# Kernel optimization log

Hardware: AMD Instinct MI355X
Metric: run time of the kernel (lower is better)

The kernel has to match this reference:

```python
import jax, jax.numpy as jnp
import numpy as np

QP = 127.0          # signed symmetric 8-bit: Qp = 2**(8-1)-1
MIN_RANGE = 1e-6


def _ste_round(q):
    # round_pass: straight-through estimator round
    return q + jax.lax.stop_gradient(jnp.round(q) - q)


def _quant_per_token(x):
    # symmetric per-token: amax over last dim, keepdim
    s = jnp.clip(jnp.max(jnp.abs(x), axis=-1, keepdims=True), MIN_RANGE, None) / QP
    return _ste_round(x / s), s


def _quant_per_tensor(w):
    s = jnp.clip(jnp.max(jnp.abs(w)), MIN_RANGE, None) / QP
    return _ste_round(w / s), s


def _qlinear(x2d, w, b):
    # fake-quant linear: quantize act per-token, weight per-tensor,
    # int-domain matmul, bias added before dequant rescale (faithful to source)
    qx, sx = _quant_per_token(x2d)      # [N,K], [N,1]
    qw, sw = _quant_per_tensor(w)       # [M,K], scalar
    out = jnp.matmul(qx, qw.T) + b[None, :]
    return out * (sx * sw)              # [N,M]


def setup_inputs() -> dict:
    key = jax.random.key(0)
    k1, k2, k3, k4, k5 = jax.random.split(key, 5)
    B, S, D, H = 64, 197, 768, 3072
    return {
        "x": jax.random.normal(k1, (B, S, D), dtype=jnp.float32),
        "w1": jax.random.normal(k2, (H, D), dtype=jnp.float32) * 0.02,
        "b1": jax.random.normal(k3, (H,), dtype=jnp.float32) * 0.02,
        "w2": jax.random.normal(k4, (D, H), dtype=jnp.float32) * 0.02,
        "b2": jax.random.normal(k5, (D,), dtype=jnp.float32) * 0.02,
    }


def reference(x, w1, b1, w2, b2):
    B, S, D = x.shape
    x2d = x.reshape(-1, D)                         # view(-1, x.size(-1))
    h = _qlinear(x2d, w1, b1)                      # fc1
    h = jax.nn.gelu(h, approximate=False)          # ViT Mlp activation (exact GELU)
    o = _qlinear(h, w2, b2)                        # fc2
    return o.reshape(B, S, -1)
```

## Files before the change

### kernel.cpp

```cpp
#include <hip/hip_runtime.h>
#include <stdint.h>

#define QPF  127.0f
#define MINR 1e-6f

typedef int v4i __attribute__((ext_vector_type(4)));
typedef _Float16 h8 __attribute__((ext_vector_type(8)));
typedef signed char c8 __attribute__((ext_vector_type(8)));

__device__ __forceinline__ float wave_max64(float v) {
  v = fmaxf(v, __shfl_xor(v, 32, 64));
  v = fmaxf(v, __shfl_xor(v, 16, 64));
  v = fmaxf(v, __shfl_xor(v, 8, 64));
  v = fmaxf(v, __shfl_xor(v, 4, 64));
  v = fmaxf(v, __shfl_xor(v, 2, 64));
  v = fmaxf(v, __shfl_xor(v, 1, 64));
  return v;
}

__device__ __forceinline__ float gelu_exact(float x) {
  float z = fabsf(x) * 0.70710678118654752440f;
  float t = __builtin_amdgcn_rcpf(fmaf(0.3275911f, z, 1.0f));
  float p = fmaf(fmaf(fmaf(fmaf(1.061405429f, t, -1.453152027f), t,
                           1.421413741f), t, -0.284496736f), t, 0.254829592f) * t;
  float e = __expf(-z * z);
  float erfz = fmaf(-p, e, 1.0f);
  float cdf = fmaf(0.5f, copysignf(erfz, x), 0.5f);
  return x * cdf;
}

__device__ __forceinline__ void gl2lds16(const void* g, void* l) {
  __builtin_amdgcn_global_load_lds(
      (const __attribute__((address_space(1))) int*)g,
      (__attribute__((address_space(3))) int*)l,
      16, 0, 0);
}

__global__ __launch_bounds__(256) void amax2_kernel(const float* __restrict__ w1,
                                                    const float* __restrict__ w2,
                                                    int n4, unsigned* out) {
  const float4* w4 = (const float4*)(blockIdx.y ? w2 : w1);
  float m = 0.f;
  for (int i = blockIdx.x * blockDim.x + threadIdx.x; i < n4;
       i += gridDim.x * blockDim.x) {
    float4 v = w4[i];
    m = fmaxf(m, fmaxf(fmaxf(fabsf(v.x), fabsf(v.y)),
                       fmaxf(fabsf(v.z), fabsf(v.w))));
  }
  m = wave_max64(m);
  __shared__ float red[4];
  const int lane = threadIdx.x & 63, wv = threadIdx.x >> 6;
  if (lane == 0) red[wv] = m;
  __syncthreads();
  if (threadIdx.x == 0) {
    float mm = fmaxf(fmaxf(red[0], red[1]), fmaxf(red[2], red[3]));
    atomicMax(out + blockIdx.y, __float_as_uint(mm));
  }
}

__global__ __launch_bounds__(256) void wquant2_kernel(const float* __restrict__ w1,
                                                      const float* __restrict__ w2,
                                                      int n4,
                                                      const unsigned* __restrict__ amaxbits,
                                                      signed char* __restrict__ q1,
                                                      signed char* __restrict__ q2) {
  const float4* w4 = (const float4*)(blockIdx.y ? w2 : w1);
  char4* q4 = (char4*)(blockIdx.y ? q2 : q1);
  const float s = fmaxf(__uint_as_float(amaxbits[blockIdx.y]), MINR) / QPF;
  const float rs = 1.0f / s;
  for (int i = blockIdx.x * blockDim.x + threadIdx.x; i < n4;
       i += gridDim.x * blockDim.x) {
    float4 v = w4[i];
    char4 c;
    c.x = (signed char)(int)rintf(v.x * rs);
    c.y = (signed char)(int)rintf(v.y * rs);
    c.z = (signed char)(int)rintf(v.z * rs);
    c.w = (signed char)(int)rintf(v.w * rs);
    q4[i] = c;
  }
}

__global__ __launch_bounds__(64) void xquant_kernel(const float* __restrict__ x,
                                                    signed char* __restrict__ qx,
                                                    float* __restrict__ sx, int K) {
  const int token = blockIdx.x;
  const float4* xr = (const float4*)(x + (size_t)token * K);
  const int k4 = K >> 2;
  const int lane = threadIdx.x;
  float m = 0.f;
  for (int i = lane; i < k4; i += 64) {
    float4 v = xr[i];
    m = fmaxf(m, fmaxf(fmaxf(fabsf(v.x), fabsf(v.y)),
                       fmaxf(fabsf(v.z), fabsf(v.w))));
  }
  m = wave_max64(m);
  const float s = fmaxf(m, MINR) / QPF;
  const float rs = 1.0f / s;
  if (lane == 0) sx[token] = s;
  char4* qr = (char4*)(qx + (size_t)token * K);
  for (int i = lane; i < k4; i += 64) {
    float4 v = xr[i];
    char4 c;
    c.x = (signed char)(int)rintf(v.x * rs);
    c.y = (signed char)(int)rintf(v.y * rs);
    c.z = (signed char)(int)rintf(v.z * rs);
    c.w = (signed char)(int)rintf(v.w * rs);
    qr[i] = c;
  }
}

__global__ __launch_bounds__(64) void hquant_kernel(const _Float16* __restrict__ h,
                                                    const unsigned* __restrict__ amaxbits,
                                                    signed char* __restrict__ qh,
                                                    float* __restrict__ sh, int K) {
  const int token = blockIdx.x;
  const float s = fmaxf(__uint_as_float(amaxbits[token]), MINR) / QPF;
  const float rs = 1.0f / s;
  if (threadIdx.x == 0) sh[token] = s;
  const h8* hr = (const h8*)(h + (size_t)token * K);
  c8* qr = (c8*)(qh + (size_t)token * K);
  for (int i = threadIdx.x; i < (K >> 3); i += 64) {
    h8 v = hr[i];
    c8 c;
#pragma unroll
    for (int j = 0; j < 8; j++)
      c[j] = (signed char)(int)rintf((float)v[j] * rs);
    qr[i] = c;
  }
}

template <bool GELU_EPI>
__global__ __launch_bounds__(256, 2) void gemm_i8(
    const signed char* __restrict__ A,
    const signed char* __restrict__ B,
    const float* __restrict__ bias,
    const float* __restrict__ sA,
    const unsigned* __restrict__ sBbits,
    void* __restrict__ outv,
    unsigned* __restrict__ amax_out,
    int N, int K, int Mout) {
  __shared__ __align__(16) signed char lds[3 * 16384];

  const int t = threadIdx.x;
  const int lane = t & 63;
  const int wv = t >> 6;
  const int wm = wv >> 1;
  const int wn = wv & 1;
  const int rowBlk = blockIdx.y * 128;
  const int colBlk = blockIdx.x * 128;

  int ar0 = rowBlk + wv * 16 + (lane >> 2);
  int ar1 = ar0 + 64;
  if (ar0 > N - 1) ar0 = N - 1;
  if (ar1 > N - 1) ar1 = N - 1;
  const int br0 = colBlk + wv * 16 + (lane >> 2);
  const int br1 = br0 + 64;
  const int kb = (((lane & 3) ^ ((lane >> 3) & 3)) * 16);

  const signed char* gA0 = A + (size_t)ar0 * K + kb;
  const signed char* gA1 = A + (size_t)ar1 * K + kb;
  const signed char* gB0 = B + (size_t)br0 * K + kb;
  const signed char* gB1 = B + (size_t)br1 * K + kb;

  const v4i vzero = {0, 0, 0, 0};
  v4i acc[4][4];
#pragma unroll
  for (int i = 0; i < 4; i++)
#pragma unroll
    for (int j = 0; j < 4; j++) acc[i][j] = vzero;

  const int swz = ((lane >> 4) ^ ((lane >> 1) & 3)) * 16;
  const int aoff = (wm * 64 + (lane & 15)) * 64 + swz;
  const int boff = (wn * 64 + (lane & 15)) * 64 + swz + 8192;

  const int T = K >> 6;

  auto issue = [&](int bufo) {
    signed char* a = lds + bufo + wv * 1024;
    gl2lds16(gA0, a);
    gl2lds16(gA1, a + 4096);
    gl2lds16(gB0, a + 8192);
    gl2lds16(gB1, a + 12288);
    gA0 += 64; gA1 += 64; gB0 += 64; gB1 += 64;
  };

  issue(0);
  if (T > 1) issue(16384);

  int cur = 0;
  for (int kt = 0; kt < T; ++kt) {
    asm volatile("" ::: "memory");
    if (kt < T - 1)
      __builtin_amdgcn_s_waitcnt(0x0074);
    else
      __builtin_amdgcn_s_waitcnt(0x0070);
    __builtin_amdgcn_s_barrier();
    asm volatile("" ::: "memory");

    if (kt + 2 < T) {
      int pf = cur + 32768;
      if (pf >= 49152) pf -= 49152;
      issue(pf);
    }

    v4i a[4], b[4];
#pragma unroll
    for (int mi = 0; mi < 4; mi++)
      a[mi] = *(const v4i*)(lds + cur + aoff + mi * 1024);
#pragma unroll
    for (int ni = 0; ni < 4; ni++)
      b[ni] = *(const v4i*)(lds + cur + boff + ni * 1024);
#pragma unroll
    for (int mi = 0; mi < 4; mi++)
#pragma unroll
      for (int ni = 0; ni < 4; ni++)
        acc[mi][ni] = __builtin_amdgcn_mfma_i32_16x16x64_i8(a[mi], b[ni],
                                                            acc[mi][ni], 0, 0, 0);
    cur += 16384;
    if (cur >= 49152) cur = 0;
  }

  const float sB = fmaxf(__uint_as_float(*sBbits), MINR) / QPF;
  const int colb = colBlk + wn * 64 + (lane & 15);
  const int rowb = rowBlk + wm * 64 + (lane >> 4) * 4;

  float bv[4];
#pragma unroll
  for (int ni = 0; ni < 4; ni++) bv[ni] = bias[colb + ni * 16];

#pragma unroll
  for (int mi = 0; mi < 4; mi++) {
    const int row0 = rowb + mi * 16;
    float sAv[4];
#pragma unroll
    for (int r = 0; r < 4; r++) sAv[r] = (row0 + r < N) ? sA[row0 + r] : 0.f;
    float rmax[4] = {0.f, 0.f, 0.f, 0.f};
#pragma unroll
    for (int ni = 0; ni < 4; ni++) {
#pragma unroll
      for (int r = 0; r < 4; r++) {
        float v = ((float)acc[mi][ni][r] + bv[ni]) * (sAv[r] * sB);
        if (GELU_EPI) v = gelu_exact(v);
        rmax[r] = fmaxf(rmax[r], fabsf(v));
        if (row0 + r < N) {
          const size_t idx = (size_t)(row0 + r) * Mout + colb + ni * 16;
          if (GELU_EPI)
            ((_Float16*)outv)[idx] = (_Float16)v;
          else
            ((float*)outv)[idx] = v;
        }
      }
    }
    if (GELU_EPI) {
#pragma unroll
      for (int r = 0; r < 4; r++) {
        float m = rmax[r];
        m = fmaxf(m, __shfl_xor(m, 1, 64));
        m = fmaxf(m, __shfl_xor(m, 2, 64));
        m = fmaxf(m, __shfl_xor(m, 4, 64));
        m = fmaxf(m, __shfl_xor(m, 8, 64));
        if ((lane & 15) == 0 && row0 + r < N)
          atomicMax(amax_out + row0 + r, __float_as_uint(m));
      }
    }
  }
}

extern "C" void kernel_launch(void* const* d_in, const int* in_sizes, int n_in,
                              void* d_out, int out_size, void* d_ws, size_t ws_size,
                              hipStream_t stream) {
  const float* x  = (const float*)d_in[0];
  const float* w1 = (const float*)d_in[1];
  const float* b1 = (const float*)d_in[2];
  const float* w2 = (const float*)d_in[3];
  const float* b2 = (const float*)d_in[4];

  const int H = in_sizes[2];
  const int D = in_sizes[4];
  const int N = in_sizes[0] / D;
  float* out = (float*)d_out;

  char* ws = (char*)d_ws;
  auto alloc = [&](size_t bytes) {
    char* p = ws;
    ws += (bytes + 255) & ~(size_t)255;
    return p;
  };
  signed char* qx  = (signed char*)alloc((size_t)N * D);
  signed char* qw1 = (signed char*)alloc((size_t)H * D);
  signed char* qw2 = (signed char*)alloc((size_t)H * D);
  signed char* qh  = (signed char*)alloc((size_t)N * H);
  float*    sx     = (float*)alloc((size_t)N * 4);
  float*    sh     = (float*)alloc((size_t)N * 4);
  unsigned* amaxh  = (unsigned*)alloc((size_t)N * 4);
  unsigned* wamax  = (unsigned*)alloc(256);
  _Float16* h      = (_Float16*)alloc((size_t)N * H * 2);
  (void)ws_size;

  hipMemsetAsync(amaxh, 0, (((size_t)N * 4 + 255) & ~(size_t)255) + 256, stream);

  const int n4w = (H * D) >> 2;
  amax2_kernel<<<dim3(512, 2), 256, 0, stream>>>(w1, w2, n4w, wamax);
  wquant2_kernel<<<dim3(1024, 2), 256, 0, stream>>>(w1, w2, n4w, wamax, qw1, qw2);
  xquant_kernel<<<N, 64, 0, stream>>>(x, qx, sx, D);

  dim3 g1(H / 128, (N + 127) / 128);
  gemm_i8<true><<<g1, 256, 0, stream>>>(qx, qw1, b1, sx, wamax + 0, (void*)h,
                                        amaxh, N, D, H);
  hquant_kernel<<<N, 64, 0, stream>>>(h, amaxh, qh, sh, H);

  dim3 g2(D / 128, (N + 127) / 128);
  gemm_i8<false><<<g2, 256, 0, stream>>>(qh, qw2, b2, sh, wamax + 1, (void*)out,
                                         nullptr, N, H, D);
}
```

Before: 266.3 us.

## Fuse preprocessing kernels, stage GEMM epilogues via LDS, retile second GEMM

```diff
diff --git a/kernel.cpp b/kernel.cpp
--- a/kernel.cpp
+++ b/kernel.cpp
@@ -36,40 +36,77 @@
       16, 0, 0);
 }
 
-__global__ __launch_bounds__(256) void amax2_kernel(const float* __restrict__ w1,
-                                                    const float* __restrict__ w2,
-                                                    int n4, unsigned* out) {
-  const float4* w4 = (const float4*)(blockIdx.y ? w2 : w1);
-  float m = 0.f;
-  for (int i = blockIdx.x * blockDim.x + threadIdx.x; i < n4;
-       i += gridDim.x * blockDim.x) {
-    float4 v = w4[i];
-    m = fmaxf(m, fmaxf(fmaxf(fabsf(v.x), fabsf(v.y)),
-                       fmaxf(fabsf(v.z), fabsf(v.w))));
-  }
+__global__ __launch_bounds__(256) void pre_kernel(
+    const float* __restrict__ w1, const float* __restrict__ w2, int n4,
+    const float* __restrict__ x, signed char* __restrict__ qx,
+    float* __restrict__ sx, unsigned* __restrict__ amaxh,
+    float* __restrict__ partial, int K, int nTok) {
+  __shared__ float red[4];
+  const int b = blockIdx.x;
+  const int tid = threadIdx.x;
+  const int lane = tid & 63, wvi = tid >> 6;
+
+  if (b < 1024) {
+    const float4* w4 = (const float4*)(b < 512 ? w1 : w2);
+    const int bb = b & 511;
+    float m = 0.f;
+    for (int i = bb * 256 + tid; i < n4; i += 512 * 256) {
+      float4 v = w4[i];
+      m = fmaxf(m, fmaxf(fmaxf(fabsf(v.x), fabsf(v.y)),
+                         fmaxf(fabsf(v.z), fabsf(v.w))));
+    }
+    m = wave_max64(m);
+    if (lane == 0) red[wvi] = m;
+    __syncthreads();
+    if (tid == 0)
+      partial[b] = fmaxf(fmaxf(red[0], red[1]), fmaxf(red[2], red[3]));
+  } else {
+    const int token = b - 1024;
+    const float4* xr = (const float4*)(x + (size_t)token * K);
+    const int k4 = K >> 2;
+    float m = 0.f;
+    float4 v = {0.f, 0.f, 0.f, 0.f};
+    if (tid < k4) {
+      v = xr[tid];
+      m = fmaxf(fmaxf(fabsf(v.x), fabsf(v.y)), fmaxf(fabsf(v.z), fabsf(v.w)));
+    }
+    m = wave_max64(m);
+    if (lane == 0) red[wvi] = m;
+    __syncthreads();
+    const float M = fmaxf(fmaxf(red[0], red[1]), fmaxf(red[2], red[3]));
+    const float s = fmaxf(M, MINR) / QPF;
+    const float rs = 1.0f / s;
+    if (tid == 0) { sx[token] = s; amaxh[token] = 0u; }
+    if (tid < k4) {
+      char4 c;
+      c.x = (signed char)(int)rintf(v.x * rs);
+      c.y = (signed char)(int)rintf(v.y * rs);
+      c.z = (signed char)(int)rintf(v.z * rs);
+      c.w = (signed char)(int)rintf(v.w * rs);
+      ((char4*)(qx + (size_t)token * K))[tid] = c;
+    }
+  }
+}
+
+__global__ __launch_bounds__(256) void wquant2_kernel(
+    const float* __restrict__ w1, const float* __restrict__ w2, int n4,
+    const float* __restrict__ partial, unsigned* __restrict__ wamax,
+    signed char* __restrict__ q1, signed char* __restrict__ q2) {
+  __shared__ float red[4];
+  const int tid = threadIdx.x;
+  const int lane = tid & 63, wvi = tid >> 6;
+  const int y = blockIdx.y;
+  float m = fmaxf(partial[y * 512 + tid], partial[y * 512 + 256 + tid]);
   m = wave_max64(m);
-  __shared__ float red[4];
-  const int lane = threadIdx.x & 63, wv = threadIdx.x >> 6;
-  if (lane == 0) red[wv] = m;
+  if (lane == 0) red[wvi] = m;
   __syncthreads();
-  if (threadIdx.x == 0) {
-    float mm = fmaxf(fmaxf(red[0], red[1]), fmaxf(red[2], red[3]));
-    atomicMax(out + blockIdx.y, __float_as_uint(mm));
-  }
-}
-
-__global__ __launch_bounds__(256) void wquant2_kernel(const float* __restrict__ w1,
-                                                      const float* __restrict__ w2,
-                                                      int n4,
-                                                      const unsigned* __restrict__ amaxbits,
-                                                      signed char* __restrict__ q1,
-                                                      signed char* __restrict__ q2) {
-  const float4* w4 = (const float4*)(blockIdx.y ? w2 : w1);
-  char4* q4 = (char4*)(blockIdx.y ? q2 : q1);
-  const float s = fmaxf(__uint_as_float(amaxbits[blockIdx.y]), MINR) / QPF;
+  const float M = fmaxf(fmaxf(red[0], red[1]), fmaxf(red[2], red[3]));
+  if (blockIdx.x == 0 && tid == 0) wamax[y] = __float_as_uint(M);
+  const float s = fmaxf(M, MINR) / QPF;
   const float rs = 1.0f / s;
-  for (int i = blockIdx.x * blockDim.x + threadIdx.x; i < n4;
-       i += gridDim.x * blockDim.x) {
+  const float4* w4 = (const float4*)(y ? w2 : w1);
+  char4* q4 = (char4*)(y ? q2 : q1);
+  for (int i = blockIdx.x * 256 + tid; i < n4; i += gridDim.x * 256) {
     float4 v = w4[i];
     char4 c;
     c.x = (signed char)(int)rintf(v.x * rs);
@@ -80,46 +117,17 @@
   }
 }
 
-__global__ __launch_bounds__(64) void xquant_kernel(const float* __restrict__ x,
-                                                    signed char* __restrict__ qx,
-                                                    float* __restrict__ sx, int K) {
-  const int token = blockIdx.x;
-  const float4* xr = (const float4*)(x + (size_t)token * K);
-  const int k4 = K >> 2;
-  const int lane = threadIdx.x;
-  float m = 0.f;
-  for (int i = lane; i < k4; i += 64) {
-    float4 v = xr[i];
-    m = fmaxf(m, fmaxf(fmaxf(fabsf(v.x), fabsf(v.y)),
-                       fmaxf(fabsf(v.z), fabsf(v.w))));
-  }
-  m = wave_max64(m);
-  const float s = fmaxf(m, MINR) / QPF;
-  const float rs = 1.0f / s;
-  if (lane == 0) sx[token] = s;
-  char4* qr = (char4*)(qx + (size_t)token * K);
-  for (int i = lane; i < k4; i += 64) {
-    float4 v = xr[i];
-    char4 c;
-    c.x = (signed char)(int)rintf(v.x * rs);
-    c.y = (signed char)(int)rintf(v.y * rs);
-    c.z = (signed char)(int)rintf(v.z * rs);
-    c.w = (signed char)(int)rintf(v.w * rs);
-    qr[i] = c;
-  }
-}
-
-__global__ __launch_bounds__(64) void hquant_kernel(const _Float16* __restrict__ h,
-                                                    const unsigned* __restrict__ amaxbits,
-                                                    signed char* __restrict__ qh,
-                                                    float* __restrict__ sh, int K) {
-  const int token = blockIdx.x;
+__global__ __launch_bounds__(256) void hquant4_kernel(
+    const _Float16* __restrict__ h, const unsigned* __restrict__ amaxbits,
+    signed char* __restrict__ qh, float* __restrict__ sh, int K) {
+  const int token = blockIdx.x * 4 + (threadIdx.x >> 6);
+  const int lane = threadIdx.x & 63;
   const float s = fmaxf(__uint_as_float(amaxbits[token]), MINR) / QPF;
   const float rs = 1.0f / s;
-  if (threadIdx.x == 0) sh[token] = s;
+  if (lane == 0) sh[token] = s;
   const h8* hr = (const h8*)(h + (size_t)token * K);
   c8* qr = (c8*)(qh + (size_t)token * K);
-  for (int i = threadIdx.x; i < (K >> 3); i += 64) {
+  for (int i = lane; i < (K >> 3); i += 64) {
     h8 v = hr[i];
     c8 c;
 #pragma unroll
@@ -129,16 +137,11 @@
   }
 }
 
-template <bool GELU_EPI>
-__global__ __launch_bounds__(256, 2) void gemm_i8(
-    const signed char* __restrict__ A,
-    const signed char* __restrict__ B,
-    const float* __restrict__ bias,
-    const float* __restrict__ sA,
-    const unsigned* __restrict__ sBbits,
-    void* __restrict__ outv,
-    unsigned* __restrict__ amax_out,
-    int N, int K, int Mout) {
+__global__ __launch_bounds__(256, 2) void gemm1_i8(
+    const signed char* __restrict__ A, const signed char* __restrict__ B,
+    const float* __restrict__ bias, const float* __restrict__ sA,
+    const unsigned* __restrict__ sBbits, _Float16* __restrict__ out,
+    unsigned* __restrict__ amax_out, int N, int K, int Mout) {
   __shared__ __align__(16) signed char lds[3 * 16384];
 
   const int t = threadIdx.x;
@@ -185,7 +188,7 @@
   };
 
   issue(0);
-  if (T > 1) issue(16384);
+  issue(16384);
 
   int cur = 0;
   for (int kt = 0; kt < T; ++kt) {
@@ -221,47 +224,180 @@
   }
 
   const float sB = fmaxf(__uint_as_float(*sBbits), MINR) / QPF;
-  const int colb = colBlk + wn * 64 + (lane & 15);
-  const int rowb = rowBlk + wm * 64 + (lane >> 4) * 4;
+  const int colb = wn * 64 + (lane & 15);
+  const int rowb = wm * 64 + (lane >> 4) * 4;
 
   float bv[4];
 #pragma unroll
-  for (int ni = 0; ni < 4; ni++) bv[ni] = bias[colb + ni * 16];
+  for (int ni = 0; ni < 4; ni++) bv[ni] = bias[colBlk + colb + ni * 16];
+
+  __syncthreads();
+  _Float16* Hs = (_Float16*)lds;
 
 #pragma unroll
   for (int mi = 0; mi < 4; mi++) {
-    const int row0 = rowb + mi * 16;
+    const int lrow0 = rowb + mi * 16;
+    const int grow0 = rowBlk + lrow0;
     float sAv[4];
 #pragma unroll
-    for (int r = 0; r < 4; r++) sAv[r] = (row0 + r < N) ? sA[row0 + r] : 0.f;
+    for (int r = 0; r < 4; r++) sAv[r] = (grow0 + r < N) ? sA[grow0 + r] : 0.f;
     float rmax[4] = {0.f, 0.f, 0.f, 0.f};
 #pragma unroll
     for (int ni = 0; ni < 4; ni++) {
 #pragma unroll
       for (int r = 0; r < 4; r++) {
         float v = ((float)acc[mi][ni][r] + bv[ni]) * (sAv[r] * sB);
-        if (GELU_EPI) v = gelu_exact(v);
+        v = gelu_exact(v);
         rmax[r] = fmaxf(rmax[r], fabsf(v));
-        if (row0 + r < N) {
-          const size_t idx = (size_t)(row0 + r) * Mout + colb + ni * 16;
-          if (GELU_EPI)
-            ((_Float16*)outv)[idx] = (_Float16)v;
-          else
-            ((float*)outv)[idx] = v;
-        }
+        Hs[(lrow0 + r) * 136 + colb + ni * 16] = (_Float16)v;
       }
     }
-    if (GELU_EPI) {
-#pragma unroll
-      for (int r = 0; r < 4; r++) {
-        float m = rmax[r];
-        m = fmaxf(m, __shfl_xor(m, 1, 64));
-        m = fmaxf(m, __shfl_xor(m, 2, 64));
-        m = fmaxf(m, __shfl_xor(m, 4, 64));
-        m = fmaxf(m, __shfl_xor(m, 8, 64));
-        if ((lane & 15) == 0 && row0 + r < N)
-          atomicMax(amax_out + row0 + r, __float_as_uint(m));
-      }
+#pragma unroll
+    for (int r = 0; r < 4; r++) {
+      float m = rmax[r];
+      m = fmaxf(m, __shfl_xor(m, 1, 64));
+      m = fmaxf(m, __shfl_xor(m, 2, 64));
+      m = fmaxf(m, __shfl_xor(m, 4, 64));
+      m = fmaxf(m, __shfl_xor(m, 8, 64));
+      if ((lane & 15) == 0 && grow0 + r < N)
+        atomicMax(amax_out + grow0 + r, __float_as_uint(m));
+    }
+  }
+  __syncthreads();
+  {
+    const int r = t >> 1, hh = t & 1;
+    const int grow = rowBlk + r;
+    if (grow < N) {
+      const v4i* src = (const v4i*)((const signed char*)lds + r * 272 + hh * 128);
+      v4i* dst = (v4i*)(out + (size_t)grow * Mout + colBlk + hh * 64);
+#pragma unroll
+      for (int j = 0; j < 8; j++) dst[j] = src[j];
+    }
+  }
+}
+
+__global__ __launch_bounds__(128, 2) void gemm2_i8(
+    const signed char* __restrict__ A, const signed char* __restrict__ B,
+    const float* __restrict__ bias, const float* __restrict__ sA,
+    const unsigned* __restrict__ sBbits, float* __restrict__ out,
+    int N, int K, int Mout) {
+  __shared__ __align__(16) signed char lds[3 * 12288];
+
+  const int t = threadIdx.x;
+  const int lane = t & 63;
+  const int wv = t >> 6;
+  const int rowBlk = blockIdx.y * 128;
+  const int colBlk = blockIdx.x * 64;
+
+  const int trow = t >> 2;
+  const int kb = (((t & 3) ^ ((t >> 3) & 3)) * 16);
+
+  int ar[4];
+#pragma unroll
+  for (int i = 0; i < 4; i++) {
+    ar[i] = rowBlk + i * 32 + trow;
+    if (ar[i] > N - 1) ar[i] = N - 1;
+  }
+  const signed char* gA0 = A + (size_t)ar[0] * K + kb;
+  const signed char* gA1 = A + (size_t)ar[1] * K + kb;
+  const signed char* gA2 = A + (size_t)ar[2] * K + kb;
+  const signed char* gA3 = A + (size_t)ar[3] * K + kb;
+  const signed char* gB0 = B + (size_t)(colBlk + trow) * K + kb;
+  const signed char* gB1 = B + (size_t)(colBlk + 32 + trow) * K + kb;
+
+  const v4i vzero = {0, 0, 0, 0};
+  v4i acc[4][4];
+#pragma unroll
+  for (int i = 0; i < 4; i++)
+#pragma unroll
+    for (int j = 0; j < 4; j++) acc[i][j] = vzero;
+
+  const int swz = ((lane >> 4) ^ ((lane >> 1) & 3)) * 16;
+  const int aoff = (wv * 64 + (lane & 15)) * 64 + swz;
+  const int boff = 8192 + (lane & 15) * 64 + swz;
+
+  const int T = K >> 6;
+
+  auto issue = [&](int bufo) {
+    signed char* p = lds + bufo + t * 16;
+    gl2lds16(gA0, p);
+    gl2lds16(gA1, p + 2048);
+    gl2lds16(gA2, p + 4096);
+    gl2lds16(gA3, p + 6144);
+    gl2lds16(gB0, p + 8192);
+    gl2lds16(gB1, p + 10240);
+    gA0 += 64; gA1 += 64; gA2 += 64; gA3 += 64; gB0 += 64; gB1 += 64;
+  };
+
+  issue(0);
+  issue(12288);
+
+  int cur = 0;
+  for (int kt = 0; kt < T; ++kt) {
+    asm volatile("" ::: "memory");
+    if (kt < T - 1)
+      __builtin_amdgcn_s_waitcnt(0x0076);
+    else
+      __builtin_amdgcn_s_waitcnt(0x0070);
+    __builtin_amdgcn_s_barrier();
+    asm volatile("" ::: "memory");
+
+    if (kt + 2 < T) {
+      int pf = cur + 24576;
+      if (pf >= 36864) pf -= 36864;
+      issue(pf);
+    }
+
+    v4i a[4], b[4];
+#pragma unroll
+    for (int mi = 0; mi < 4; mi++)
+      a[mi] = *(const v4i*)(lds + cur + aoff + mi * 1024);
+#pragma unroll
+    for (int ni = 0; ni < 4; ni++)
+      b[ni] = *(const v4i*)(lds + cur + boff + ni * 1024);
+#pragma unroll
+    for (int mi = 0; mi < 4; mi++)
+#pragma unroll
+      for (int ni = 0; ni < 4; ni++)
+        acc[mi][ni] = __builtin_amdgcn_mfma_i32_16x16x64_i8(a[mi], b[ni],
+                                                            acc[mi][ni], 0, 0, 0);
+    cur += 12288;
+    if (cur >= 36864) cur = 0;
+  }
+
+  const float sB = fmaxf(__uint_as_float(*sBbits), MINR) / QPF;
+  const int colb = lane & 15;
+  const int rowb = wv * 64 + (lane >> 4) * 4;
+
+  float bv[4];
+#pragma unroll
+  for (int ni = 0; ni < 4; ni++) bv[ni] = bias[colBlk + colb + ni * 16];
+
+  __syncthreads();
+  float* Cs = (float*)lds;
+
+#pragma unroll
+  for (int mi = 0; mi < 4; mi++) {
+    const int lrow0 = rowb + mi * 16;
+    const int grow0 = rowBlk + lrow0;
+    float sAv[4];
+#pragma unroll
+    for (int r = 0; r < 4; r++) sAv[r] = (grow0 + r < N) ? sA[grow0 + r] : 0.f;
+#pragma unroll
+    for (int ni = 0; ni < 4; ni++)
+#pragma unroll
+      for (int r = 0; r < 4; r++)
+        Cs[(lrow0 + r) * 66 + colb + ni * 16] =
+            ((float)acc[mi][ni][r] + bv[ni]) * (sAv[r] * sB);
+  }
+  __syncthreads();
+  {
+    const int grow = rowBlk + t;
+    if (grow < N) {
+      const v4i* src = (const v4i*)(Cs + t * 66);
+      v4i* dst = (v4i*)(out + (size_t)grow * Mout + colBlk);
+#pragma unroll
+      for (int j = 0; j < 16; j++) dst[j] = src[j];
     }
   }
 }
@@ -294,22 +430,22 @@
   float*    sh     = (float*)alloc((size_t)N * 4);
   unsigned* amaxh  = (unsigned*)alloc((size_t)N * 4);
   unsigned* wamax  = (unsigned*)alloc(256);
+  float*    partial= (float*)alloc(1024 * 4);
   _Float16* h      = (_Float16*)alloc((size_t)N * H * 2);
   (void)ws_size;
 
-  hipMemsetAsync(amaxh, 0, (((size_t)N * 4 + 255) & ~(size_t)255) + 256, stream);
-
   const int n4w = (H * D) >> 2;
-  amax2_kernel<<<dim3(512, 2), 256, 0, stream>>>(w1, w2, n4w, wamax);
-  wquant2_kernel<<<dim3(1024, 2), 256, 0, stream>>>(w1, w2, n4w, wamax, qw1, qw2);
-  xquant_kernel<<<N, 64, 0, stream>>>(x, qx, sx, D);
+
+  pre_kernel<<<1024 + N, 256, 0, stream>>>(w1, w2, n4w, x, qx, sx, amaxh,
+                                           partial, D, N);
+  wquant2_kernel<<<dim3(512, 2), 256, 0, stream>>>(w1, w2, n4w, partial, wamax,
+                                                   qw1, qw2);
 
   dim3 g1(H / 128, (N + 127) / 128);
-  gemm_i8<true><<<g1, 256, 0, stream>>>(qx, qw1, b1, sx, wamax + 0, (void*)h,
-                                        amaxh, N, D, H);
-  hquant_kernel<<<N, 64, 0, stream>>>(h, amaxh, qh, sh, H);
-
-  dim3 g2(D / 128, (N + 127) / 128);
-  gemm_i8<false><<<g2, 256, 0, stream>>>(qh, qw2, b2, sh, wamax + 1, (void*)out,
-                                         nullptr, N, H, D);
-}
+  gemm1_i8<<<g1, 256, 0, stream>>>(qx, qw1, b1, sx, wamax + 0, h, amaxh,
+                                   N, D, H);
+  hquant4_kernel<<<N / 4, 256, 0, stream>>>(h, amaxh, qh, sh, H);
+
+  dim3 g2(D / 64, (N + 127) / 128);
+  gemm2_i8<<<g2, 128, 0, stream>>>(qh, qw2, b2, sh, wamax + 1, out, N, H, D);
+}
```

Result: slower. 281.2 us (+5.6%).
